# Kernel tuning notes

Measured on AMD Instinct MI355X. Metric: run time of the kernel, lower is better.

Reference implementation:

```python
import jax, jax.numpy as jnp
import numpy as np

B, T, D, DL, E, H, K = 4, 2048, 1024, 128, 8, 4, 3
HD = DL // H


def setup_inputs() -> dict:
    key = jax.random.key(0)
    ks = jax.random.split(key, 12)
    s = jnp.float32(0.02)
    f = lambda k, shape: jax.random.normal(k, shape, dtype=jnp.float32)
    zeros = lambda n: jnp.zeros((n,), jnp.float32)
    ones = lambda n: jnp.ones((n,), jnp.float32)
    return {
        "x": f(ks[0], (B, T, D)),
        "w_down": f(ks[1], (E * DL, D)) * s,
        "expert_pos_embed": f(ks[2], (1, E, DL)) * s,
        "global_proj_w": f(ks[3], (DL, D)) * s,
        "global_proj_b": zeros(DL),
        "attn_in_w": f(ks[4], (3 * DL, DL)) * s,
        "attn_in_b": zeros(3 * DL),
        "attn_out_w": f(ks[5], (DL, DL)) * s,
        "attn_out_b": zeros(DL),
        "norm_w": ones(DL),
        "norm_b": zeros(DL),
        "rq1_w": f(ks[6], (DL, DL)) * s,
        "rq1_b": zeros(DL),
        "rq_ln_w": ones(DL),
        "rq_ln_b": zeros(DL),
        "rq2_w": f(ks[7], (DL, DL)) * s,
        "rq2_b": zeros(DL),
        "rk_w": f(ks[8], (DL, DL)) * s,
        "rk_b": zeros(DL),
        "w_up": f(ks[9], (E, DL, D)) * s,
    }


def _ln(x, w, b):
    m = jnp.mean(x, axis=-1, keepdims=True)
    v = jnp.mean((x - m) ** 2, axis=-1, keepdims=True)
    return (x - m) * jax.lax.rsqrt(v + 1e-5) * w + b


def _gelu(x):
    return jax.nn.gelu(x, approximate=False)  # torch nn.GELU() default is exact erf


def reference(x, w_down, expert_pos_embed, global_proj_w, global_proj_b,
              attn_in_w, attn_in_b, attn_out_w, attn_out_b, norm_w, norm_b,
              rq1_w, rq1_b, rq_ln_w, rq_ln_b, rq2_w, rq2_b, rk_w, rk_b, w_up):
    N = B * T
    xf = x.reshape(N, D)
    expert_feats = (xf @ w_down.T).reshape(N, E, DL)  # [N,E,DL]
    # global context, broadcast to every token as a length-1 query
    gctx = x.mean(axis=1) @ global_proj_w.T + global_proj_b  # [B,DL]
    gctx = jnp.broadcast_to(gctx[:, None, :], (B, T, DL)).reshape(N, 1, DL)
    # 9-token (1 global + E experts) self-attention round table
    seq = jnp.concatenate([gctx, expert_feats + expert_pos_embed], axis=1)  # [N,E+1,DL]
    qkv = seq @ attn_in_w.T + attn_in_b
    q, k, v = jnp.split(qkv, 3, axis=-1)
    split_heads = lambda t: t.reshape(N, E + 1, H, HD).transpose(0, 2, 1, 3)
    q, k, v = split_heads(q), split_heads(k), split_heads(v)
    attn = jax.nn.softmax(jnp.einsum('nhqd,nhkd->nhqk', q, k) / jnp.sqrt(jnp.float32(HD)), axis=-1)
    o = jnp.einsum('nhqk,nhkd->nhqd', attn, v).transpose(0, 2, 1, 3).reshape(N, E + 1, DL)
    o = o @ attn_out_w.T + attn_out_b
    seq2 = _ln(o + seq, norm_w, norm_b)
    refined = seq2[:, 1:, :]  # [N,E,DL]
    # routing: refined expert keys vs projected global query
    rq = _gelu(_ln(gctx[:, 0, :] @ rq1_w.T + rq1_b, rq_ln_w, rq_ln_b)) @ rq2_w.T + rq2_b  # [N,DL]
    rk = refined @ rk_w.T + rk_b  # [N,E,DL]
    logits = jnp.einsum('nd,ned->ne', rq, rk) / jnp.sqrt(jnp.float32(DL))
    probs = jax.nn.softmax(logits, axis=-1)
    tw, ti = jax.lax.top_k(probs, K)
    tw = tw / tw.sum(axis=-1, keepdims=True)
    # expert up-projection; computing all E then gathering top-k outputs is
    # mathematically identical to gathering w_up[indices] first, but avoids
    # materializing the [N,K,DL,D] duplicated weight tensor
    all_out = jnp.einsum('ned,edm->nem', _gelu(expert_feats), w_up)  # [N,E,D]
    sel_out = jnp.take_along_axis(all_out, ti[:, :, None], axis=1)  # [N,K,D]
    weighted = jnp.sum(sel_out * tw[:, :, None], axis=1)  # [N,D]
    # aux load-balance loss
    mean_prob = probs.mean(axis=0)
    one_hot = jnp.zeros((N, E), probs.dtype).at[jnp.arange(N)[:, None], ti].set(1.0)
    mean_load = one_hot.mean(axis=0)
    aux_loss = E * jnp.sum(mean_prob * mean_load)
    return weighted.reshape(B, T, D), aux_loss
```

## Files before the change

### kernel.cpp

```cpp
#include <hip/hip_runtime.h>
#include <hip/hip_bf16.h>
#include <math.h>

#define BB 4
#define TT 2048
#define DD 1024
#define DLb 128
#define EE 8
#define HH 4
#define KK 3
#define HDh 32
#define NN (BB*TT)
#define NPOS 9
#define NCH 16
#define CHL (TT/NCH)
#define SEQSTR (NPOS*DLb)
#define NSLICE 4
#define TSL (NN/NSLICE)

typedef __attribute__((ext_vector_type(8))) short short8;
typedef __attribute__((ext_vector_type(4))) float f32x4;
typedef __attribute__((ext_vector_type(8))) unsigned short ushort8;
typedef __attribute__((ext_vector_type(4))) unsigned short ushort4v;

#define GLL(gptr, lptr) \
    __builtin_amdgcn_global_load_lds((const __attribute__((address_space(1))) unsigned int*)(gptr), \
                                     (__attribute__((address_space(3))) unsigned int*)(lptr), 16, 0, 0)

__device__ __forceinline__ float gelu_exact(float v) {
    return 0.5f * v * (1.0f + erff(v * 0.70710678118654752440f));
}

__device__ __forceinline__ unsigned short f2bf(float x) {
    __hip_bfloat16 h = __float2bfloat16(x);
    return *reinterpret_cast<unsigned short*>(&h);
}

__device__ __forceinline__ float bf2f(unsigned short u) {
    return __uint_as_float(((unsigned int)u) << 16);
}

__device__ __forceinline__ float4 rec4(const unsigned short* h, const unsigned short* l) {
    ushort4v hv = *(const ushort4v*)h;
    ushort4v lv = *(const ushort4v*)l;
    float4 r;
    r.x = bf2f(hv[0]) + bf2f(lv[0]);
    r.y = bf2f(hv[1]) + bf2f(lv[1]);
    r.z = bf2f(hv[2]) + bf2f(lv[2]);
    r.w = bf2f(hv[3]) + bf2f(lv[3]);
    return r;
}

__device__ __forceinline__ void stage_panel(const unsigned short* __restrict__ G,
                                            size_t rowBase, int L, int k0,
                                            unsigned short* lds, int tid)
{
    int r = tid >> 2, c8 = (tid & 3) * 8;
    int wave = tid >> 6;
    GLL(&G[(rowBase + r) * (size_t)L + k0 + c8], lds + wave * 512);
    GLL(&G[(rowBase + 64 + r) * (size_t)L + k0 + c8], lds + 2048 + wave * 512);
}

__global__ __launch_bounds__(256) void ksplit(const float* __restrict__ src,
                                              unsigned short* __restrict__ h,
                                              unsigned short* __restrict__ l, int n8)
{
    int i = blockIdx.x * 256 + threadIdx.x;
    if (i >= n8) return;
    size_t g = (size_t)i * 8;
    float4 a = *(const float4*)&src[g];
    float4 b = *(const float4*)&src[g + 4];
    float vv[8] = {a.x, a.y, a.z, a.w, b.x, b.y, b.z, b.w};
    ushort8 ho, lo;
    #pragma unroll
    for (int j = 0; j < 8; j++) {
        unsigned short hh = f2bf(vv[j]);
        float hf = bf2f(hh);
        ho[j] = hh;
        lo[j] = f2bf(vv[j] - hf);
    }
    *(ushort8*)&h[g] = ho;
    *(ushort8*)&l[g] = lo;
}

__global__ __launch_bounds__(256) void k1a(const float* __restrict__ x, float* __restrict__ partial) {
    int d = blockIdx.x * 256 + threadIdx.x;
    int b = blockIdx.y, c = blockIdx.z;
    const float* xp = x + ((size_t)b * TT + (size_t)c * CHL) * DD + d;
    float s = 0.0f;
    for (int t = 0; t < CHL; t++) s += xp[(size_t)t * DD];
    partial[(b * NCH + c) * DD + d] = s;
}

__global__ __launch_bounds__(256) void k1b(const float* __restrict__ partial, float* __restrict__ mean_x) {
    int d = blockIdx.x * 256 + threadIdx.x;
    int b = blockIdx.y;
    float s = 0.0f;
    for (int c = 0; c < NCH; c++) s += partial[(b * NCH + c) * DD + d];
    mean_x[b * DD + d] = s * (1.0f / TT);
}

__global__ __launch_bounds__(128) void k2_batch(
    const float* __restrict__ mean_x,
    const float* __restrict__ gpw, const float* __restrict__ gpb,
    const float* __restrict__ rq1w, const float* __restrict__ rq1b,
    const float* __restrict__ lnw, const float* __restrict__ lnb,
    const float* __restrict__ rq2w, const float* __restrict__ rq2b,
    const float* __restrict__ rkw, const float* __restrict__ rkb,
    float* __restrict__ gctx, float* __restrict__ uv, float* __restrict__ c0v)
{
    int b = blockIdx.x, d = threadIdx.x;
    __shared__ __attribute__((aligned(16))) float g[DLb];
    __shared__ __attribute__((aligned(16))) float t1[DLb];
    __shared__ __attribute__((aligned(16))) float act[DLb];
    __shared__ __attribute__((aligned(16))) float rqs[DLb];
    __shared__ float red[2];
    {
        const float4* wrow = (const float4*)(gpw + (size_t)d * DD);
        const float4* mx4  = (const float4*)(mean_x + (size_t)b * DD);
        float s = gpb[d];
        for (int k = 0; k < DD / 4; k++) {
            float4 w = wrow[k], m = mx4[k];
            s += w.x * m.x + w.y * m.y + w.z * m.z + w.w * m.w;
        }
        g[d] = s;
        gctx[b * DLb + d] = s;
    }
    __syncthreads();
    {
        float s = rq1b[d];
        for (int k = 0; k < DLb; k++) s += g[k] * rq1w[d * DLb + k];
        t1[d] = s;
    }
    __syncthreads();
    if (d == 0) {
        float m = 0.0f;
        for (int i = 0; i < DLb; i++) m += t1[i];
        m *= (1.0f / DLb);
        float v = 0.0f;
        for (int i = 0; i < DLb; i++) { float df = t1[i] - m; v += df * df; }
        v *= (1.0f / DLb);
        red[0] = m; red[1] = 1.0f / sqrtf(v + 1e-5f);
    }
    __syncthreads();
    {
        float xn = (t1[d] - red[0]) * red[1] * lnw[d] + lnb[d];
        act[d] = gelu_exact(xn);
    }
    __syncthreads();
    {
        float s = rq2b[d];
        for (int k = 0; k < DLb; k++) s += act[k] * rq2w[d * DLb + k];
        rqs[d] = s;
    }
    __syncthreads();
    {
        float u = 0.0f;
        for (int k = 0; k < DLb; k++) u += rqs[k] * rkw[(size_t)k * DLb + d];
        uv[b * DLb + d] = u;
    }
    if (d == 0) {
        float c0 = 0.0f;
        for (int k = 0; k < DLb; k++) c0 += rqs[k] * rkb[k];
        c0v[b] = c0;
    }
}

__global__ __launch_bounds__(256) void k2b(const float* __restrict__ gctx,
                                           unsigned short* __restrict__ seqh,
                                           unsigned short* __restrict__ seql) {
    int i = blockIdx.x * 256 + threadIdx.x;
    int n = i >> 7, d = i & 127;
    float v = gctx[(n >> 11) * DLb + d];
    unsigned short h = f2bf(v);
    seqh[(size_t)n * SEQSTR + d] = h;
    seql[(size_t)n * SEQSTR + d] = f2bf(v - bf2f(h));
}

__global__ __launch_bounds__(256) void k3s(const unsigned short* __restrict__ XH,
                                           const unsigned short* __restrict__ XL,
                                           const unsigned short* __restrict__ WH,
                                           const unsigned short* __restrict__ WL,
                                           const float* __restrict__ pe,
                                           unsigned short* __restrict__ seqh,
                                           unsigned short* __restrict__ seql)
{
    __shared__ __attribute__((aligned(16))) unsigned short Ah[128 * 32];
    __shared__ __attribute__((aligned(16))) unsigned short Al[128 * 32];
    __shared__ __attribute__((aligned(16))) unsigned short Bh[128 * 32];
    __shared__ __attribute__((aligned(16))) unsigned short Bl[128 * 32];
    int tid = threadIdx.x;
    int lane = tid & 63, wave = tid >> 6;
    int wm = wave & 1, wn = wave >> 1;
    int row0 = blockIdx.y * 128, col0 = blockIdx.x * 128;
    int fr = lane & 15, fq = lane >> 4;
    f32x4 acc[4][4];
    #pragma unroll
    for (int i = 0; i < 4; i++)
        #pragma unroll
        for (int j = 0; j < 4; j++) acc[i][j] = (f32x4)0.0f;

    for (int k0 = 0; k0 < DD; k0 += 32) {
        stage_panel(XH, row0, DD, k0, Ah, tid);
        stage_panel(XL, row0, DD, k0, Al, tid);
        stage_panel(WH, col0, DD, k0, Bh, tid);
        stage_panel(WL, col0, DD, k0, Bl, tid);
        __syncthreads();
        short8 ah[4], al4[4], bh[4], bl4[4];
        #pragma unroll
        for (int f = 0; f < 4; f++) {
            int ra = (wm * 64 + f * 16 + fr) * 32 + fq * 8;
            int rb = (wn * 64 + f * 16 + fr) * 32 + fq * 8;
            ah[f]  = *(const short8*)&Ah[ra];
            al4[f] = *(const short8*)&Al[ra];
            bh[f]  = *(const short8*)&Bh[rb];
            bl4[f] = *(const short8*)&Bl[rb];
        }
        #pragma unroll
        for (int i = 0; i < 4; i++)
            #pragma unroll
            for (int j = 0; j < 4; j++) {
                acc[i][j] = __builtin_amdgcn_mfma_f32_16x16x32_bf16(ah[i],  bh[j],  acc[i][j], 0, 0, 0);
                acc[i][j] = __builtin_amdgcn_mfma_f32_16x16x32_bf16(ah[i],  bl4[j], acc[i][j], 0, 0, 0);
                acc[i][j] = __builtin_amdgcn_mfma_f32_16x16x32_bf16(al4[i], bh[j],  acc[i][j], 0, 0, 0);
            }
        __syncthreads();
    }
    #pragma unroll
    for (int j = 0; j < 4; j++) {
        int gc = col0 + wn * 64 + j * 16 + fr;
        float pv = pe[gc];
        #pragma unroll
        for (int i = 0; i < 4; i++) {
            #pragma unroll
            for (int r = 0; r < 4; r++) {
                int gr = row0 + wm * 64 + i * 16 + fq * 4 + r;
                float v = acc[i][j][r] + pv;
                unsigned short h = f2bf(v);
                size_t idx = (size_t)gr * SEQSTR + DLb + gc;
                seqh[idx] = h;
                seql[idx] = f2bf(v - bf2f(h));
            }
        }
    }
}

__global__ __launch_bounds__(256) void k4as(const unsigned short* __restrict__ AHp,
                                            const unsigned short* __restrict__ ALp,
                                            const unsigned short* __restrict__ WHp,
                                            const unsigned short* __restrict__ WLp,
                                            const float* __restrict__ bias,
                                            float* __restrict__ C)
{
    __shared__ __attribute__((aligned(16))) unsigned short Ah[128 * 32];
    __shared__ __attribute__((aligned(16))) unsigned short Al[128 * 32];
    __shared__ __attribute__((aligned(16))) unsigned short Bh[128 * 32];
    __shared__ __attribute__((aligned(16))) unsigned short Bl[128 * 32];
    int tid = threadIdx.x;
    int lane = tid & 63, wave = tid >> 6;
    int wm = wave & 1, wn = wave >> 1;
    int row0 = blockIdx.y * 128, col0 = blockIdx.x * 128;
    int fr = lane & 15, fq = lane >> 4;
    f32x4 acc[4][4];
    #pragma unroll
    for (int i = 0; i < 4; i++)
        #pragma unroll
        for (int j = 0; j < 4; j++) acc[i][j] = (f32x4)0.0f;

    for (int k0 = 0; k0 < DLb; k0 += 32) {
        stage_panel(AHp, row0, DLb, k0, Ah, tid);
        stage_panel(ALp, row0, DLb, k0, Al, tid);
        stage_panel(WHp, col0, DLb, k0, Bh, tid);
        stage_panel(WLp, col0, DLb, k0, Bl, tid);
        __syncthreads();
        short8 ah[4], al4[4], bh[4], bl4[4];
        #pragma unroll
        for (int f = 0; f < 4; f++) {
            int ra = (wm * 64 + f * 16 + fr) * 32 + fq * 8;
            int rb = (wn * 64 + f * 16 + fr) * 32 + fq * 8;
            ah[f]  = *(const short8*)&Ah[ra];
            al4[f] = *(const short8*)&Al[ra];
            bh[f]  = *(const short8*)&Bh[rb];
            bl4[f] = *(const short8*)&Bl[rb];
        }
        #pragma unroll
        for (int i = 0; i < 4; i++)
            #pragma unroll
            for (int j = 0; j < 4; j++) {
                acc[i][j] = __builtin_amdgcn_mfma_f32_16x16x32_bf16(ah[i],  bh[j],  acc[i][j], 0, 0, 0);
                acc[i][j] = __builtin_amdgcn_mfma_f32_16x16x32_bf16(ah[i],  bl4[j], acc[i][j], 0, 0, 0);
                acc[i][j] = __builtin_amdgcn_mfma_f32_16x16x32_bf16(al4[i], bh[j],  acc[i][j], 0, 0, 0);
            }
        __syncthreads();
    }
    #pragma unroll
    for (int j = 0; j < 4; j++) {
        int gc = col0 + wn * 64 + j * 16 + fr;
        float bv = bias[gc];
        #pragma unroll
        for (int i = 0; i < 4; i++) {
            #pragma unroll
            for (int r = 0; r < 4; r++) {
                int gr = row0 + wm * 64 + i * 16 + fq * 4 + r;
                C[(size_t)gr * 384 + gc] = acc[i][j][r] + bv;
            }
        }
    }
}

__global__ __launch_bounds__(256) void k4b(const float* __restrict__ qkv,
                                           float* __restrict__ og, int n0)
{
    int nl = blockIdx.x;
    int tid = threadIdx.x;
    __shared__ __attribute__((aligned(16))) float sq[NPOS][384];
    __shared__ float attnw[HH][NPOS][12];
    {
        const float4* src = (const float4*)(qkv + (size_t)nl * NPOS * 384);
        float4* dst = (float4*)&sq[0][0];
        for (int i = tid; i < NPOS * 384 / 4; i += 256) dst[i] = src[i];
    }
    __syncthreads();
    if (tid < HH * NPOS) {
        int h = tid / NPOS, i = tid % NPOS;
        float sc[NPOS];
        float mx = -1e30f;
        for (int j = 0; j < NPOS; j++) {
            float s = 0.0f;
            for (int d2 = 0; d2 < HDh; d2++)
                s += sq[i][h * HDh + d2] * sq[j][DLb + h * HDh + d2];
            s *= 0.17677669529663687f;
            sc[j] = s;
            mx = fmaxf(mx, s);
        }
        float se = 0.0f;
        for (int j = 0; j < NPOS; j++) { sc[j] = expf(sc[j] - mx); se += sc[j]; }
        float inv = 1.0f / se;
        for (int j = 0; j < NPOS; j++) attnw[h][i][j] = sc[j] * inv;
    }
    __syncthreads();
    #pragma unroll
    for (int it = 0; it < 4; it++) {
        int idx = it * 256 + tid;
        int p = 1 + (idx >> 7), d = idx & 127, h = d >> 5;
        float s = 0.0f;
        #pragma unroll
        for (int j = 0; j < NPOS; j++) s += attnw[h][p][j] * sq[j][2 * DLb + d];
        og[((size_t)(n0 + nl) * 8 + (p - 1)) * DLb + d] = s;
    }
}

__global__ __launch_bounds__(256) void k4cd(const float* __restrict__ A,
                                            const float* __restrict__ W,
                                            const float* __restrict__ bias,
                                            const unsigned short* __restrict__ seqh,
                                            const unsigned short* __restrict__ seql,
                                            const float* __restrict__ nw,
                                            const float* __restrict__ nb,
                                            const float* __restrict__ uv,
                                            const float* __restrict__ c0v,
                                            float* __restrict__ logits)
{
    __shared__ __attribute__((aligned(16))) float As[16][132];
    __shared__ __attribute__((aligned(16))) float Bs[16][132];
    __shared__ float redS[128][17];
    __shared__ float mstat[128][2];
    int tid = threadIdx.x;
    int tx = tid & 15, ty = tid >> 4;
    int row0 = blockIdx.y * 128;
    float acc[8][8] = {};
    for (int k0 = 0; k0 < DLb; k0 += 16) {
        #pragma unroll
        for (int i = 0; i < 2; i++) {
            int L = i * 256 + tid;
            int r = L >> 2, kq = (L & 3) * 4;
            float4 a4 = *(const float4*)&A[(size_t)(row0 + r) * DLb + k0 + kq];
            float4 b4 = *(const float4*)&W[(size_t)r * DLb + k0 + kq];
            As[kq + 0][r] = a4.x; As[kq + 1][r] = a4.y; As[kq + 2][r] = a4.z; As[kq + 3][r] = a4.w;
            Bs[kq + 0][r] = b4.x; Bs[kq + 1][r] = b4.y; Bs[kq + 2][r] = b4.z; Bs[kq + 3][r] = b4.w;
        }
        __syncthreads();
        #pragma unroll
        for (int kk = 0; kk < 16; kk++) {
            float4 a0 = *(const float4*)&As[kk][ty * 4];
            float4 a1 = *(const float4*)&As[kk][64 + ty * 4];
            float4 b0 = *(const float4*)&Bs[kk][tx * 4];
            float4 b1 = *(const float4*)&Bs[kk][64 + tx * 4];
            float ar[8] = {a0.x, a0.y, a0.z, a0.w, a1.x, a1.y, a1.z, a1.w};
            float bc[8] = {b0.x, b0.y, b0.z, b0.w, b1.x, b1.y, b1.z, b1.w};
            #pragma unroll
            for (int i = 0; i < 8; i++)
                #pragma unroll
                for (int j = 0; j < 8; j++)
                    acc[i][j] += ar[i] * bc[j];
        }
        __syncthreads();
    }
    int b = row0 >> 14;
    float4 bb0 = *(const float4*)&bias[tx * 4];
    float4 bb1 = *(const float4*)&bias[64 + tx * 4];
    #pragma unroll
    for (int i = 0; i < 8; i++) {
        int rl = (i < 4) ? (ty * 4 + i) : (64 + ty * 4 + (i - 4));
        int m = row0 + rl;
        size_t roff = (size_t)(m >> 3) * SEQSTR + (size_t)((m & 7) + 1) * DLb;
        float4 r0 = rec4(&seqh[roff + tx * 4], &seql[roff + tx * 4]);
        float4 r1 = rec4(&seqh[roff + 64 + tx * 4], &seql[roff + 64 + tx * 4]);
        acc[i][0] += bb0.x + r0.x; acc[i][1] += bb0.y + r0.y;
        acc[i][2] += bb0.z + r0.z; acc[i][3] += bb0.w + r0.w;
        acc[i][4] += bb1.x + r1.x; acc[i][5] += bb1.y + r1.y;
        acc[i][6] += bb1.z + r1.z; acc[i][7] += bb1.w + r1.w;
        float ps = 0.0f;
        #pragma unroll
        for (int j = 0; j < 8; j++) ps += acc[i][j];
        redS[rl][tx] = ps;
    }
    __syncthreads();
    if (tid < 128) {
        float s = 0.0f;
        #pragma unroll
        for (int t = 0; t < 16; t++) s += redS[tid][t];
        mstat[tid][0] = s * (1.0f / DLb);
    }
    __syncthreads();
    #pragma unroll
    for (int i = 0; i < 8; i++) {
        int rl = (i < 4) ? (ty * 4 + i) : (64 + ty * 4 + (i - 4));
        float m = mstat[rl][0];
        float pv = 0.0f;
        #pragma unroll
        for (int j = 0; j < 8; j++) { float df = acc[i][j] - m; pv += df * df; }
        redS[rl][tx] = pv;
    }
    __syncthreads();
    if (tid < 128) {
        float s = 0.0f;
        #pragma unroll
        for (int t = 0; t < 16; t++) s += redS[tid][t];
        mstat[tid][1] = 1.0f / sqrtf(s * (1.0f / DLb) + 1e-5f);
    }
    __syncthreads();
    const float* u = uv + b * DLb;
    float4 nw0 = *(const float4*)&nw[tx * 4];
    float4 nw1 = *(const float4*)&nw[64 + tx * 4];
    float4 nb0 = *(const float4*)&nb[tx * 4];
    float4 nb1 = *(const float4*)&nb[64 + tx * 4];
    float4 u0 = *(const float4*)&u[tx * 4];
    float4 u1 = *(const float4*)&u[64 + tx * 4];
    #pragma unroll
    for (int i = 0; i < 8; i++) {
        int rl = (i < 4) ? (ty * 4 + i) : (64 + ty * 4 + (i - 4));
        float m = mstat[rl][0], istd = mstat[rl][1];
        float ps;
        ps  = ((acc[i][0] - m) * istd * nw0.x + nb0.x) * u0.x;
        ps += ((acc[i][1] - m) * istd * nw0.y + nb0.y) * u0.y;
        ps += ((acc[i][2] - m) * istd * nw0.z + nb0.z) * u0.z;
        ps += ((acc[i][3] - m) * istd * nw0.w + nb0.w) * u0.w;
        ps += ((acc[i][4] - m) * istd * nw1.x + nb1.x) * u1.x;
        ps += ((acc[i][5] - m) * istd * nw1.y + nb1.y) * u1.y;
        ps += ((acc[i][6] - m) * istd * nw1.z + nb1.z) * u1.z;
        ps += ((acc[i][7] - m) * istd * nw1.w + nb1.w) * u1.w;
        redS[rl][tx] = ps;
    }
    __syncthreads();
    if (tid < 128) {
        float s = 0.0f;
        #pragma unroll
        for (int t = 0; t < 16; t++) s += redS[tid][t];
        logits[row0 + tid] = (s + c0v[b]) * 0.08838834764831845f;
    }
}

__global__ __launch_bounds__(256) void k4e(const float* __restrict__ logits,
                                           float* __restrict__ probs,
                                           float* __restrict__ wsel)
{
    int n = blockIdx.x * 256 + threadIdx.x;
    if (n >= NN) return;
    float lg[EE];
    float4 l0 = *(const float4*)&logits[(size_t)n * EE];
    float4 l1 = *(const float4*)&logits[(size_t)n * EE + 4];
    lg[0] = l0.x; lg[1] = l0.y; lg[2] = l0.z; lg[3] = l0.w;
    lg[4] = l1.x; lg[5] = l1.y; lg[6] = l1.z; lg[7] = l1.w;
    float mx = lg[0];
    #pragma unroll
    for (int e = 1; e < EE; e++) mx = fmaxf(mx, lg[e]);
    float pr[EE];
    float se = 0.0f;
    #pragma unroll
    for (int e = 0; e < EE; e++) { pr[e] = expf(lg[e] - mx); se += pr[e]; }
    float inv = 1.0f / se;
    #pragma unroll
    for (int e = 0; e < EE; e++) pr[e] *= inv;
    float4 p0, p1;
    p0.x = pr[0]; p0.y = pr[1]; p0.z = pr[2]; p0.w = pr[3];
    p1.x = pr[4]; p1.y = pr[5]; p1.z = pr[6]; p1.w = pr[7];
    *(float4*)&probs[(size_t)n * EE] = p0;
    *(float4*)&probs[(size_t)n * EE + 4] = p1;
    bool used[EE] = {};
    int sel[KK];
    float sw = 0.0f;
    for (int t = 0; t < KK; t++) {
        int bi = 0; float bv = -1e30f;
        for (int e = 0; e < EE; e++)
            if (!used[e] && pr[e] > bv) { bv = pr[e]; bi = e; }
        used[bi] = true; sel[t] = bi; sw += pr[bi];
    }
    float invsw = 1.0f / sw;
    float w8[EE];
    #pragma unroll
    for (int e = 0; e < EE; e++) w8[e] = 0.0f;
    for (int t = 0; t < KK; t++) w8[sel[t]] = pr[sel[t]] * invsw;
    float4 w0, w1;
    w0.x = w8[0]; w0.y = w8[1]; w0.z = w8[2]; w0.w = w8[3];
    w1.x = w8[4]; w1.y = w8[5]; w1.z = w8[6]; w1.w = w8[7];
    *(float4*)&wsel[(size_t)n * EE] = w0;
    *(float4*)&wsel[(size_t)n * EE + 4] = w1;
}

__global__ __launch_bounds__(256) void k5pre(const unsigned short* __restrict__ seqh,
                                             const unsigned short* __restrict__ seql,
                                             const float* __restrict__ pe,
                                             const float* __restrict__ wsel,
                                             unsigned short* __restrict__ abf)
{
    size_t g = ((size_t)blockIdx.x * 256 + threadIdx.x) * 8;
    int n = (int)(g >> 10), k0 = (int)(g & 1023);
    int e = k0 >> 7;
    float w = wsel[(size_t)n * EE + e];
    size_t soff = (size_t)n * SEQSTR + DLb + k0;
    ushort8 hv = *(const ushort8*)&seqh[soff];
    ushort8 lv = *(const ushort8*)&seql[soff];
    float4 p0 = *(const float4*)&pe[k0];
    float4 p1 = *(const float4*)&pe[k0 + 4];
    float pp[8] = {p0.x, p0.y, p0.z, p0.w, p1.x, p1.y, p1.z, p1.w};
    ushort8 o;
    #pragma unroll
    for (int i = 0; i < 8; i++) {
        float v = bf2f(hv[i]) + bf2f(lv[i]) - pp[i];
        o[i] = f2bf(w * gelu_exact(v));
    }
    *(ushort8*)&abf[g] = o;
}

__global__ __launch_bounds__(256) void k5t(const float* __restrict__ wup, unsigned short* __restrict__ wupT) {
    __shared__ float T[64][68];
    int tid = threadIdx.x;
    int k0 = blockIdx.x * 64, m0 = blockIdx.y * 64;
    #pragma unroll
    for (int i = 0; i < 4; i++) {
        int F = i * 256 + tid;
        int r = F >> 4, c4 = (F & 15) * 4;
        *(float4*)&T[r][c4] = *(const float4*)&wup[(size_t)(k0 + r) * DD + m0 + c4];
    }
    __syncthreads();
    #pragma unroll
    for (int i = 0; i < 2; i++) {
        int W = i * 256 + tid;
        int r = W >> 3, c8 = (W & 7) * 8;
        ushort8 o;
        #pragma unroll
        for (int j = 0; j < 8; j++) o[j] = f2bf(T[c8 + j][r]);
        *(ushort8*)&wupT[(size_t)(m0 + r) * DD + k0 + c8] = o;
    }
}

__global__ __launch_bounds__(256) void k5_mfma(const unsigned short* __restrict__ A,
                                               const unsigned short* __restrict__ B,
                                               float* __restrict__ C)
{
    __shared__ __attribute__((aligned(16))) unsigned short As[128 * 32];
    __shared__ __attribute__((aligned(16))) unsigned short Bs[128 * 32];
    int tid = threadIdx.x;
    int lane = tid & 63, wave = tid >> 6;
    int wm = wave & 1, wn = wave >> 1;
    int row0 = blockIdx.y * 128, col0 = blockIdx.x * 128;
    int fr = lane & 15, fq = lane >> 4;
    f32x4 acc[4][4];
    #pragma unroll
    for (int i = 0; i < 4; i++)
        #pragma unroll
        for (int j = 0; j < 4; j++) acc[i][j] = (f32x4)0.0f;

    for (int k0 = 0; k0 < DD; k0 += 32) {
        stage_panel(A, row0, DD, k0, As, tid);
        stage_panel(B, col0, DD, k0, Bs, tid);
        __syncthreads();
        short8 af[4], bf[4];
        #pragma unroll
        for (int f = 0; f < 4; f++) {
            af[f] = *(const short8*)&As[(wm * 64 + f * 16 + fr) * 32 + fq * 8];
            bf[f] = *(const short8*)&Bs[(wn * 64 + f * 16 + fr) * 32 + fq * 8];
        }
        #pragma unroll
        for (int i = 0; i < 4; i++)
            #pragma unroll
            for (int j = 0; j < 4; j++)
                acc[i][j] = __builtin_amdgcn_mfma_f32_16x16x32_bf16(af[i], bf[j], acc[i][j], 0, 0, 0);
        __syncthreads();
    }
    #pragma unroll
    for (int i = 0; i < 4; i++) {
        #pragma unroll
        for (int j = 0; j < 4; j++) {
            int gc = col0 + wn * 64 + j * 16 + fr;
            #pragma unroll
            for (int r = 0; r < 4; r++) {
                int gr = row0 + wm * 64 + i * 16 + fq * 4 + r;
                C[(size_t)gr * DD + gc] = acc[i][j][r];
            }
        }
    }
}

__global__ __launch_bounds__(256) void k6a(const float* __restrict__ probs,
                                           const float* __restrict__ wsel,
                                           float* __restrict__ part)
{
    int tid = threadIdx.x;
    int n = blockIdx.x * 256 + tid;
    float lp[EE], lc[EE];
    #pragma unroll
    for (int e = 0; e < EE; e++) {
        lp[e] = probs[(size_t)n * EE + e];
        lc[e] = (wsel[(size_t)n * EE + e] > 0.0f) ? 1.0f : 0.0f;
    }
    __shared__ float bp[256][EE];
    __shared__ float bc[256][EE];
    #pragma unroll
    for (int e = 0; e < EE; e++) { bp[tid][e] = lp[e]; bc[tid][e] = lc[e]; }
    __syncthreads();
    for (int s = 128; s > 0; s >>= 1) {
        if (tid < s) {
            #pragma unroll
            for (int e = 0; e < EE; e++) {
                bp[tid][e] += bp[tid + s][e];
                bc[tid][e] += bc[tid + s][e];
            }
        }
        __syncthreads();
    }
    if (tid < EE) {
        part[blockIdx.x * 16 + tid] = bp[0][tid];
        part[blockIdx.x * 16 + 8 + tid] = bc[0][tid];
    }
}

__global__ __launch_bounds__(64) void k6b(const float* __restrict__ part, float* __restrict__ out_aux) {
    int tid = threadIdx.x;
    __shared__ float sums[16];
    if (tid < 16) {
        float s = 0.0f;
        for (int b = 0; b < NN / 256; b++) s += part[b * 16 + tid];
        sums[tid] = s;
    }
    __syncthreads();
    if (tid == 0) {
        float a = 0.0f;
        for (int e = 0; e < EE; e++) a += (sums[e] / NN) * (sums[8 + e] / NN);
        out_aux[0] = EE * a;
    }
}

extern "C" void kernel_launch(void* const* d_in, const int* in_sizes, int n_in,
                              void* d_out, int out_size, void* d_ws, size_t ws_size,
                              hipStream_t stream) {
    const float* x     = (const float*)d_in[0];
    const float* wdown = (const float*)d_in[1];
    const float* pe    = (const float*)d_in[2];
    const float* gpw   = (const float*)d_in[3];
    const float* gpb   = (const float*)d_in[4];
    const float* aiw   = (const float*)d_in[5];
    const float* aib   = (const float*)d_in[6];
    const float* aow   = (const float*)d_in[7];
    const float* aob   = (const float*)d_in[8];
    const float* nw    = (const float*)d_in[9];
    const float* nb    = (const float*)d_in[10];
    const float* rq1w  = (const float*)d_in[11];
    const float* rq1b  = (const float*)d_in[12];
    const float* rqlnw = (const float*)d_in[13];
    const float* rqlnb = (const float*)d_in[14];
    const float* rq2w  = (const float*)d_in[15];
    const float* rq2b  = (const float*)d_in[16];
    const float* rkw   = (const float*)d_in[17];
    const float* rkb   = (const float*)d_in[18];
    const float* wup   = (const float*)d_in[19];

    float* out = (float*)d_out;

    unsigned short* seqh = (unsigned short*)d_ws;
    unsigned short* seql = seqh + (size_t)NN * SEQSTR;
    float* xregion = (float*)(seql + (size_t)NN * SEQSTR);
    unsigned short* xh = (unsigned short*)xregion;
    unsigned short* xl = xh + (size_t)NN * DD;
    float* o = xregion;
    unsigned short* abf = (unsigned short*)xregion;
    float* region = xregion + (size_t)NN * DD;
    float* qkvbuf = region;
    float* probs  = region + (size_t)65536 * 128;
    float* wsel   = probs + (size_t)NN * EE;
    float* logits = wsel + (size_t)NN * EE;
    float* partial= logits + (size_t)NN * EE;
    float* mean_x = partial + (size_t)BB * NCH * DD;
    float* gctx   = mean_x + (size_t)BB * DD;
    float* uv     = gctx + (size_t)BB * DLb;
    float* c0v    = uv + (size_t)BB * DLb;
    float* k6part = c0v + 64;
    unsigned short* wupT = (unsigned short*)(k6part + 512);
    unsigned short* wdh  = wupT + (size_t)DD * DD;
    unsigned short* wdl  = wdh + (size_t)DD * DD;
    unsigned short* aiwh = wdl + (size_t)DD * DD;
    unsigned short* aiwl = aiwh + (size_t)384 * DLb;

    hipLaunchKernelGGL(ksplit, dim3(NN * DD / 8 / 256), dim3(256), 0, stream, x, xh, xl, NN * DD / 8);
    hipLaunchKernelGGL(ksplit, dim3(DD * DD / 8 / 256), dim3(256), 0, stream, wdown, wdh, wdl, DD * DD / 8);
    hipLaunchKernelGGL(ksplit, dim3(384 * DLb / 8 / 256), dim3(256), 0, stream, aiw, aiwh, aiwl, 384 * DLb / 8);

    hipLaunchKernelGGL(k1a, dim3(DD / 256, BB, NCH), dim3(256), 0, stream, x, partial);
    hipLaunchKernelGGL(k1b, dim3(DD / 256, BB), dim3(256), 0, stream, partial, mean_x);
    hipLaunchKernelGGL(k2_batch, dim3(BB), dim3(DLb), 0, stream,
                       mean_x, gpw, gpb, rq1w, rq1b, rqlnw, rqlnb, rq2w, rq2b, rkw, rkb,
                       gctx, uv, c0v);
    hipLaunchKernelGGL(k2b, dim3(NN * DLb / 256), dim3(256), 0, stream, gctx, seqh, seql);
    hipLaunchKernelGGL(k3s, dim3((EE * DLb) / 128, NN / 128), dim3(256), 0, stream,
                       xh, xl, wdh, wdl, pe, seqh, seql);
    for (int s = 0; s < NSLICE; s++) {
        hipLaunchKernelGGL(k4as, dim3(3, TSL * NPOS / 128), dim3(256), 0, stream,
                           seqh + (size_t)s * TSL * SEQSTR, seql + (size_t)s * TSL * SEQSTR,
                           aiwh, aiwl, aib, qkvbuf);
        hipLaunchKernelGGL(k4b, dim3(TSL), dim3(256), 0, stream, qkvbuf, o, s * TSL);
    }
    hipLaunchKernelGGL(k4cd, dim3(1, NN * EE / 128), dim3(256), 0, stream,
                       o, aow, aob, seqh, seql, nw, nb, uv, c0v, logits);
    hipLaunchKernelGGL(k4e, dim3(NN / 256), dim3(256), 0, stream, logits, probs, wsel);
    hipLaunchKernelGGL(k5t, dim3(DD / 64, DD / 64), dim3(256), 0, stream, wup, wupT);
    hipLaunchKernelGGL(k5pre, dim3(NN * DD / (256 * 8)), dim3(256), 0, stream, seqh, seql, pe, wsel, abf);
    hipLaunchKernelGGL(k5_mfma, dim3(DD / 128, NN / 128), dim3(256), 0, stream, abf, wupT, out);
    hipLaunchKernelGGL(k6a, dim3(NN / 256), dim3(256), 0, stream, probs, wsel, k6part);
    hipLaunchKernelGGL(k6b, dim3(1), dim3(64), 0, stream, k6part, out + (size_t)NN * DD);
}
```

Measured before the change: 412.3 us.

## Use 8-wave GEMM blocks with XOR-swizzled LDS and fuse x split into mean

The three MFMA GEMM kernels move from 256 to 512 threads per block. Each wave now owns a 64x32 sub-tile, and every thread stages one 16-byte chunk per panel. The LDS layout gets an XOR swizzle on the 8-element column group, applied both when staging and when reading fragments, to cut bank conflicts. Separately, the hi/lo bf16 split of x is folded into the column-sum kernel k1a, so x is read once instead of twice. In exchange, each wave does less MFMA work per fragment load, and the k1a pass is strided by column, which may write xh/xl less efficiently.

```diff
diff --git a/kernel.cpp b/kernel.cpp
--- a/kernel.cpp
+++ b/kernel.cpp
@@ -51,14 +51,18 @@
     return r;
 }
 
-__device__ __forceinline__ void stage_panel(const unsigned short* __restrict__ G,
-                                            size_t rowBase, int L, int k0,
-                                            unsigned short* lds, int tid)
-{
-    int r = tid >> 2, c8 = (tid & 3) * 8;
-    int wave = tid >> 6;
-    GLL(&G[(rowBase + r) * (size_t)L + k0 + c8], lds + wave * 512);
-    GLL(&G[(rowBase + 64 + r) * (size_t)L + k0 + c8], lds + 2048 + wave * 512);
+__device__ __forceinline__ void stage512(const unsigned short* __restrict__ G,
+                                         size_t rowBase, int L, int k0,
+                                         unsigned short* lds, int tid)
+{
+    int r = tid >> 2;
+    int sl = tid & 3;
+    int src = sl ^ ((r >> 1) & 3);
+    GLL(&G[(rowBase + r) * (size_t)L + k0 + src * 8], lds + (tid >> 6) * 512);
+}
+
+__device__ __forceinline__ int fragoff(int row, int fq) {
+    return row * 32 + ((fq ^ ((row >> 1) & 3)) << 3);
 }
 
 __global__ __launch_bounds__(256) void ksplit(const float* __restrict__ src,
@@ -83,12 +87,21 @@
     *(ushort8*)&l[g] = lo;
 }
 
-__global__ __launch_bounds__(256) void k1a(const float* __restrict__ x, float* __restrict__ partial) {
+__global__ __launch_bounds__(256) void k1a(const float* __restrict__ x, float* __restrict__ partial,
+                                           unsigned short* __restrict__ xh,
+                                           unsigned short* __restrict__ xl) {
     int d = blockIdx.x * 256 + threadIdx.x;
     int b = blockIdx.y, c = blockIdx.z;
-    const float* xp = x + ((size_t)b * TT + (size_t)c * CHL) * DD + d;
+    size_t base = ((size_t)b * TT + (size_t)c * CHL) * DD + d;
     float s = 0.0f;
-    for (int t = 0; t < CHL; t++) s += xp[(size_t)t * DD];
+    for (int t = 0; t < CHL; t++) {
+        size_t idx = base + (size_t)t * DD;
+        float v = x[idx];
+        s += v;
+        unsigned short h = f2bf(v);
+        xh[idx] = h;
+        xl[idx] = f2bf(v - bf2f(h));
+    }
     partial[(b * NCH + c) * DD + d] = s;
 }
 
@@ -177,13 +190,13 @@
     seql[(size_t)n * SEQSTR + d] = f2bf(v - bf2f(h));
 }
 
-__global__ __launch_bounds__(256) void k3s(const unsigned short* __restrict__ XH,
-                                           const unsigned short* __restrict__ XL,
-                                           const unsigned short* __restrict__ WH,
-                                           const unsigned short* __restrict__ WL,
-                                           const float* __restrict__ pe,
-                                           unsigned short* __restrict__ seqh,
-                                           unsigned short* __restrict__ seql)
+__global__ __launch_bounds__(512, 4) void k3s(const unsigned short* __restrict__ XH,
+                                              const unsigned short* __restrict__ XL,
+                                              const unsigned short* __restrict__ WH,
+                                              const unsigned short* __restrict__ WL,
+                                              const float* __restrict__ pe,
+                                              unsigned short* __restrict__ seqh,
+                                              unsigned short* __restrict__ seql)
 {
     __shared__ __attribute__((aligned(16))) unsigned short Ah[128 * 32];
     __shared__ __attribute__((aligned(16))) unsigned short Al[128 * 32];
@@ -194,32 +207,35 @@
     int wm = wave & 1, wn = wave >> 1;
     int row0 = blockIdx.y * 128, col0 = blockIdx.x * 128;
     int fr = lane & 15, fq = lane >> 4;
-    f32x4 acc[4][4];
+    f32x4 acc[4][2];
     #pragma unroll
     for (int i = 0; i < 4; i++)
         #pragma unroll
-        for (int j = 0; j < 4; j++) acc[i][j] = (f32x4)0.0f;
+        for (int j = 0; j < 2; j++) acc[i][j] = (f32x4)0.0f;
 
     for (int k0 = 0; k0 < DD; k0 += 32) {
-        stage_panel(XH, row0, DD, k0, Ah, tid);
-        stage_panel(XL, row0, DD, k0, Al, tid);
-        stage_panel(WH, col0, DD, k0, Bh, tid);
-        stage_panel(WL, col0, DD, k0, Bl, tid);
-        __syncthreads();
-        short8 ah[4], al4[4], bh[4], bl4[4];
+        stage512(XH, row0, DD, k0, Ah, tid);
+        stage512(XL, row0, DD, k0, Al, tid);
+        stage512(WH, col0, DD, k0, Bh, tid);
+        stage512(WL, col0, DD, k0, Bl, tid);
+        __syncthreads();
+        short8 ah[4], al4[4], bh[2], bl4[2];
         #pragma unroll
         for (int f = 0; f < 4; f++) {
-            int ra = (wm * 64 + f * 16 + fr) * 32 + fq * 8;
-            int rb = (wn * 64 + f * 16 + fr) * 32 + fq * 8;
+            int ra = fragoff(wm * 64 + f * 16 + fr, fq);
             ah[f]  = *(const short8*)&Ah[ra];
             al4[f] = *(const short8*)&Al[ra];
-            bh[f]  = *(const short8*)&Bh[rb];
-            bl4[f] = *(const short8*)&Bl[rb];
+        }
+        #pragma unroll
+        for (int g = 0; g < 2; g++) {
+            int rb = fragoff(wn * 32 + g * 16 + fr, fq);
+            bh[g]  = *(const short8*)&Bh[rb];
+            bl4[g] = *(const short8*)&Bl[rb];
         }
         #pragma unroll
         for (int i = 0; i < 4; i++)
             #pragma unroll
-            for (int j = 0; j < 4; j++) {
+            for (int j = 0; j < 2; j++) {
                 acc[i][j] = __builtin_amdgcn_mfma_f32_16x16x32_bf16(ah[i],  bh[j],  acc[i][j], 0, 0, 0);
                 acc[i][j] = __builtin_amdgcn_mfma_f32_16x16x32_bf16(ah[i],  bl4[j], acc[i][j], 0, 0, 0);
                 acc[i][j] = __builtin_amdgcn_mfma_f32_16x16x32_bf16(al4[i], bh[j],  acc[i][j], 0, 0, 0);
@@ -227,8 +243,8 @@
         __syncthreads();
     }
     #pragma unroll
-    for (int j = 0; j < 4; j++) {
-        int gc = col0 + wn * 64 + j * 16 + fr;
+    for (int j = 0; j < 2; j++) {
+        int gc = col0 + wn * 32 + j * 16 + fr;
         float pv = pe[gc];
         #pragma unroll
         for (int i = 0; i < 4; i++) {
@@ -245,12 +261,12 @@
     }
 }
 
-__global__ __launch_bounds__(256) void k4as(const unsigned short* __restrict__ AHp,
-                                            const unsigned short* __restrict__ ALp,
-                                            const unsigned short* __restrict__ WHp,
-                                            const unsigned short* __restrict__ WLp,
-                                            const float* __restrict__ bias,
-                                            float* __restrict__ C)
+__global__ __launch_bounds__(512, 4) void k4as(const unsigned short* __restrict__ AHp,
+                                               const unsigned short* __restrict__ ALp,
+                                               const unsigned short* __restrict__ WHp,
+                                               const unsigned short* __restrict__ WLp,
+                                               const float* __restrict__ bias,
+                                               float* __restrict__ C)
 {
     __shared__ __attribute__((aligned(16))) unsigned short Ah[128 * 32];
     __shared__ __attribute__((aligned(16))) unsigned short Al[128 * 32];
@@ -261,32 +277,35 @@
     int wm = wave & 1, wn = wave >> 1;
     int row0 = blockIdx.y * 128, col0 = blockIdx.x * 128;
     int fr = lane & 15, fq = lane >> 4;
-    f32x4 acc[4][4];
+    f32x4 acc[4][2];
     #pragma unroll
     for (int i = 0; i < 4; i++)
         #pragma unroll
-        for (int j = 0; j < 4; j++) acc[i][j] = (f32x4)0.0f;
+        for (int j = 0; j < 2; j++) acc[i][j] = (f32x4)0.0f;
 
     for (int k0 = 0; k0 < DLb; k0 += 32) {
-        stage_panel(AHp, row0, DLb, k0, Ah, tid);
-        stage_panel(ALp, row0, DLb, k0, Al, tid);
-        stage_panel(WHp, col0, DLb, k0, Bh, tid);
-        stage_panel(WLp, col0, DLb, k0, Bl, tid);
-        __syncthreads();
-        short8 ah[4], al4[4], bh[4], bl4[4];
+        stage512(AHp, row0, DLb, k0, Ah, tid);
+        stage512(ALp, row0, DLb, k0, Al, tid);
+        stage512(WHp, col0, DLb, k0, Bh, tid);
+        stage512(WLp, col0, DLb, k0, Bl, tid);
+        __syncthreads();
+        short8 ah[4], al4[4], bh[2], bl4[2];
         #pragma unroll
         for (int f = 0; f < 4; f++) {
-            int ra = (wm * 64 + f * 16 + fr) * 32 + fq * 8;
-            int rb = (wn * 64 + f * 16 + fr) * 32 + fq * 8;
+            int ra = fragoff(wm * 64 + f * 16 + fr, fq);
             ah[f]  = *(const short8*)&Ah[ra];
             al4[f] = *(const short8*)&Al[ra];
-            bh[f]  = *(const short8*)&Bh[rb];
-            bl4[f] = *(const short8*)&Bl[rb];
+        }
+        #pragma unroll
+        for (int g = 0; g < 2; g++) {
+            int rb = fragoff(wn * 32 + g * 16 + fr, fq);
+            bh[g]  = *(const short8*)&Bh[rb];
+            bl4[g] = *(const short8*)&Bl[rb];
         }
         #pragma unroll
         for (int i = 0; i < 4; i++)
             #pragma unroll
-            for (int j = 0; j < 4; j++) {
+            for (int j = 0; j < 2; j++) {
                 acc[i][j] = __builtin_amdgcn_mfma_f32_16x16x32_bf16(ah[i],  bh[j],  acc[i][j], 0, 0, 0);
                 acc[i][j] = __builtin_amdgcn_mfma_f32_16x16x32_bf16(ah[i],  bl4[j], acc[i][j], 0, 0, 0);
                 acc[i][j] = __builtin_amdgcn_mfma_f32_16x16x32_bf16(al4[i], bh[j],  acc[i][j], 0, 0, 0);
@@ -294,8 +313,8 @@
         __syncthreads();
     }
     #pragma unroll
-    for (int j = 0; j < 4; j++) {
-        int gc = col0 + wn * 64 + j * 16 + fr;
+    for (int j = 0; j < 2; j++) {
+        int gc = col0 + wn * 32 + j * 16 + fr;
         float bv = bias[gc];
         #pragma unroll
         for (int i = 0; i < 4; i++) {
@@ -565,9 +584,9 @@
     }
 }
 
-__global__ __launch_bounds__(256) void k5_mfma(const unsigned short* __restrict__ A,
-                                               const unsigned short* __restrict__ B,
-                                               float* __restrict__ C)
+__global__ __launch_bounds__(512, 4) void k5_mfma(const unsigned short* __restrict__ A,
+                                                  const unsigned short* __restrict__ B,
+                                                  float* __restrict__ C)
 {
     __shared__ __attribute__((aligned(16))) unsigned short As[128 * 32];
     __shared__ __attribute__((aligned(16))) unsigned short Bs[128 * 32];
@@ -576,34 +595,35 @@
     int wm = wave & 1, wn = wave >> 1;
     int row0 = blockIdx.y * 128, col0 = blockIdx.x * 128;
     int fr = lane & 15, fq = lane >> 4;
-    f32x4 acc[4][4];
+    f32x4 acc[4][2];
     #pragma unroll
     for (int i = 0; i < 4; i++)
         #pragma unroll
-        for (int j = 0; j < 4; j++) acc[i][j] = (f32x4)0.0f;
+        for (int j = 0; j < 2; j++) acc[i][j] = (f32x4)0.0f;
 
     for (int k0 = 0; k0 < DD; k0 += 32) {
-        stage_panel(A, row0, DD, k0, As, tid);
-        stage_panel(B, col0, DD, k0, Bs, tid);
-        __syncthreads();
-        short8 af[4], bf[4];
-        #pragma unroll
-        for (int f = 0; f < 4; f++) {
-            af[f] = *(const short8*)&As[(wm * 64 + f * 16 + fr) * 32 + fq * 8];
-            bf[f] = *(const short8*)&Bs[(wn * 64 + f * 16 + fr) * 32 + fq * 8];
-        }
+        stage512(A, row0, DD, k0, As, tid);
+        stage512(B, col0, DD, k0, Bs, tid);
+        __syncthreads();
+        short8 af[4], bf[2];
+        #pragma unroll
+        for (int f = 0; f < 4; f++)
+            af[f] = *(const short8*)&As[fragoff(wm * 64 + f * 16 + fr, fq)];
+        #pragma unroll
+        for (int g = 0; g < 2; g++)
+            bf[g] = *(const short8*)&Bs[fragoff(wn * 32 + g * 16 + fr, fq)];
         #pragma unroll
         for (int i = 0; i < 4; i++)
             #pragma unroll
-            for (int j = 0; j < 4; j++)
+            for (int j = 0; j < 2; j++)
                 acc[i][j] = __builtin_amdgcn_mfma_f32_16x16x32_bf16(af[i], bf[j], acc[i][j], 0, 0, 0);
         __syncthreads();
     }
     #pragma unroll
     for (int i = 0; i < 4; i++) {
         #pragma unroll
-        for (int j = 0; j < 4; j++) {
-            int gc = col0 + wn * 64 + j * 16 + fr;
+        for (int j = 0; j < 2; j++) {
+            int gc = col0 + wn * 32 + j * 16 + fr;
             #pragma unroll
             for (int r = 0; r < 4; r++) {
                 int gr = row0 + wm * 64 + i * 16 + fq * 4 + r;
@@ -712,20 +732,19 @@
     unsigned short* aiwh = wdl + (size_t)DD * DD;
     unsigned short* aiwl = aiwh + (size_t)384 * DLb;
 
-    hipLaunchKernelGGL(ksplit, dim3(NN * DD / 8 / 256), dim3(256), 0, stream, x, xh, xl, NN * DD / 8);
     hipLaunchKernelGGL(ksplit, dim3(DD * DD / 8 / 256), dim3(256), 0, stream, wdown, wdh, wdl, DD * DD / 8);
     hipLaunchKernelGGL(ksplit, dim3(384 * DLb / 8 / 256), dim3(256), 0, stream, aiw, aiwh, aiwl, 384 * DLb / 8);
 
-    hipLaunchKernelGGL(k1a, dim3(DD / 256, BB, NCH), dim3(256), 0, stream, x, partial);
+    hipLaunchKernelGGL(k1a, dim3(DD / 256, BB, NCH), dim3(256), 0, stream, x, partial, xh, xl);
     hipLaunchKernelGGL(k1b, dim3(DD / 256, BB), dim3(256), 0, stream, partial, mean_x);
     hipLaunchKernelGGL(k2_batch, dim3(BB), dim3(DLb), 0, stream,
                        mean_x, gpw, gpb, rq1w, rq1b, rqlnw, rqlnb, rq2w, rq2b, rkw, rkb,
                        gctx, uv, c0v);
     hipLaunchKernelGGL(k2b, dim3(NN * DLb / 256), dim3(256), 0, stream, gctx, seqh, seql);
-    hipLaunchKernelGGL(k3s, dim3((EE * DLb) / 128, NN / 128), dim3(256), 0, stream,
+    hipLaunchKernelGGL(k3s, dim3((EE * DLb) / 128, NN / 128), dim3(512), 0, stream,
                        xh, xl, wdh, wdl, pe, seqh, seql);
     for (int s = 0; s < NSLICE; s++) {
-        hipLaunchKernelGGL(k4as, dim3(3, TSL * NPOS / 128), dim3(256), 0, stream,
+        hipLaunchKernelGGL(k4as, dim3(3, TSL * NPOS / 128), dim3(512), 0, stream,
                            seqh + (size_t)s * TSL * SEQSTR, seql + (size_t)s * TSL * SEQSTR,
                            aiwh, aiwl, aib, qkvbuf);
         hipLaunchKernelGGL(k4b, dim3(TSL), dim3(256), 0, stream, qkvbuf, o, s * TSL);
@@ -735,7 +754,7 @@
     hipLaunchKernelGGL(k4e, dim3(NN / 256), dim3(256), 0, stream, logits, probs, wsel);
     hipLaunchKernelGGL(k5t, dim3(DD / 64, DD / 64), dim3(256), 0, stream, wup, wupT);
     hipLaunchKernelGGL(k5pre, dim3(NN * DD / (256 * 8)), dim3(256), 0, stream, seqh, seql, pe, wsel, abf);
-    hipLaunchKernelGGL(k5_mfma, dim3(DD / 128, NN / 128), dim3(256), 0, stream, abf, wupT, out);
+    hipLaunchKernelGGL(k5_mfma, dim3(DD / 128, NN / 128), dim3(512), 0, stream, abf, wupT, out);
     hipLaunchKernelGGL(k6a, dim3(NN / 256), dim3(256), 0, stream, probs, wsel, k6part);
     hipLaunchKernelGGL(k6b, dim3(1), dim3(64), 0, stream, k6part, out + (size_t)NN * DD);
 }
```

After: 407.2 us. Within noise of the previous version (-1.2%).
